# Optimization experiments

Measured on AMD Instinct MI355X. Metric: run time of the kernel, lower is better.

Reference implementation:

```python
import jax, jax.numpy as jnp
import numpy as np

NUM_HEADS = 4
NUM_GROUPS = 8
EPS = 1e-5


def setup_inputs() -> dict:
    key = jax.random.key(0)
    ks = jax.random.split(key, 4)
    b, c, h, w = 16, 512, 32, 32
    x = jax.random.normal(ks[0], (b, c, h, w), dtype=jnp.float32)
    gamma = jnp.ones((c,), dtype=jnp.float32)
    beta = jnp.zeros((c,), dtype=jnp.float32)
    # conv1d kernel-size-1 weights expressed as [out, in] matrices
    w_qkv = jax.random.normal(ks[1], (3 * c, c), dtype=jnp.float32) * (1.0 / np.sqrt(c))
    b_qkv = jnp.zeros((3 * c,), dtype=jnp.float32)
    w_proj = jax.random.normal(ks[2], (c, c), dtype=jnp.float32) * (1.0 / np.sqrt(c))
    b_proj = jnp.zeros((c,), dtype=jnp.float32)
    return {"x": x, "gamma": gamma, "beta": beta, "w_qkv": w_qkv,
            "b_qkv": b_qkv, "w_proj": w_proj, "b_proj": b_proj}


def group_norm(x, gamma, beta):
    # x: [b, c, h, w]; normalize per (group) over (c/g, h, w)
    b, c, h, w = x.shape
    xg = x.reshape(b, NUM_GROUPS, c // NUM_GROUPS, h, w)
    mean = xg.mean(axis=(2, 3, 4), keepdims=True)
    var = xg.var(axis=(2, 3, 4), keepdims=True)
    xn = ((xg - mean) * jax.lax.rsqrt(var + EPS)).reshape(b, c, h, w)
    return xn * gamma[None, :, None, None] + beta[None, :, None, None]


def reference(x, gamma, beta, w_qkv, b_qkv, w_proj, b_proj):
    b, c, h, w = x.shape
    L = h * w
    hd = c // NUM_HEADS  # head_dim
    x_in = x
    xn = group_norm(x, gamma, beta).reshape(b, c, L)
    # 1x1 conv == matmul over channel dim: [b, 3c, L]
    qkv = jnp.einsum('oc,bcl->bol', w_qkv, xn) + b_qkv[None, :, None]
    q, k, v = jnp.split(qkv, 3, axis=1)  # each [b, c, L]
    q = q.reshape(b, NUM_HEADS, hd, L)
    k = k.reshape(b, NUM_HEADS, hd, L)
    v = v.reshape(b, NUM_HEADS, hd, L)
    scale = hd ** (-0.5)
    attn = jnp.einsum('bhdl,bhdm->bhlm', q * scale, k)  # [b,h,L,L]
    attn = jax.nn.softmax(attn, axis=-1)
    out = jnp.einsum('bhlm,bhdm->bhdl', attn, v).reshape(b, c, L)
    out = jnp.einsum('oc,bcl->bol', w_proj, out) + b_proj[None, :, None]
    return x_in + out.reshape(b, c, h, w)
```

## Files before the change

kernel.cpp:

```cpp
#include <hip/hip_runtime.h>
#include <hip/hip_bf16.h>

typedef __hip_bfloat16 bf16;
typedef __attribute__((ext_vector_type(8))) short short8;
typedef __attribute__((ext_vector_type(4))) float f32x4;
typedef __attribute__((ext_vector_type(16))) float f32x16;

__device__ __forceinline__ float b2f(bf16 v) { return __bfloat162float(v); }
__device__ __forceinline__ bf16  f2b(float v) { return __float2bfloat16(v); }

__global__ __launch_bounds__(256) void convert_w_kernel(
    const float* __restrict__ wq, const float* __restrict__ wp,
    bf16* __restrict__ wqb, bf16* __restrict__ wpb)
{
    int ch = blockIdx.x * 256 + threadIdx.x;
    float4 v;
    bf16* dst;
    if (ch < 196608) {
        v = ((const float4*)wq)[ch];
        dst = wqb + ch * 4;
    } else {
        int c2 = ch - 196608;
        v = ((const float4*)wp)[c2];
        dst = wpb + c2 * 4;
    }
    bf16 o[4] = {f2b(v.x), f2b(v.y), f2b(v.z), f2b(v.w)};
    *(uint2*)dst = *(const uint2*)o;
}

__global__ __launch_bounds__(256) void gn_partial_kernel(
    const float* __restrict__ x,
    float* __restrict__ partS, float* __restrict__ partQ)
{
    const int bid = blockIdx.x;
    const size_t base = (size_t)bid * 16384;
    const int t = threadIdx.x;

    float sum = 0.f, ssq = 0.f;
    const float4* x4 = (const float4*)(x + base);
    for (int i = t; i < 4096; i += 256) {
        float4 v = x4[i];
        sum += v.x + v.y + v.z + v.w;
        ssq += v.x * v.x + v.y * v.y + v.z * v.z + v.w * v.w;
    }
    #pragma unroll
    for (int off = 32; off > 0; off >>= 1) {
        sum += __shfl_down(sum, off);
        ssq += __shfl_down(ssq, off);
    }
    __shared__ float red[8];
    const int wid = t >> 6, lane = t & 63;
    if (lane == 0) { red[wid] = sum; red[4 + wid] = ssq; }
    __syncthreads();
    if (t == 0) {
        partS[bid] = red[0] + red[1] + red[2] + red[3];
        partQ[bid] = red[4] + red[5] + red[6] + red[7];
    }
}

__global__ __launch_bounds__(64) void gn_finalize_kernel(
    const float* __restrict__ partS, const float* __restrict__ partQ,
    const float* __restrict__ gamma, const float* __restrict__ beta,
    float* __restrict__ scaleB, float* __restrict__ shiftB)
{
    const int bg = blockIdx.x;
    const int b = bg >> 3, g = bg & 7;
    const int t = threadIdx.x;
    float s = partS[bg * 4] + partS[bg * 4 + 1] + partS[bg * 4 + 2] + partS[bg * 4 + 3];
    float q = partQ[bg * 4] + partQ[bg * 4 + 1] + partQ[bg * 4 + 2] + partQ[bg * 4 + 3];
    float mean = s * (1.f / 65536.f);
    float var  = q * (1.f / 65536.f) - mean * mean;
    float rstd = rsqrtf(var + 1e-5f);
    int c = g * 64 + t;
    float sc = rstd * gamma[c];
    scaleB[b * 512 + c] = sc;
    shiftB[b * 512 + c] = beta[c] - mean * sc;
}

__global__ __launch_bounds__(256) void gn_apply_t_kernel(
    const float* __restrict__ x,
    const float* __restrict__ scaleB,
    const float* __restrict__ shiftB,
    bf16* __restrict__ Xt)
{
    const int lt = blockIdx.x, ct = blockIdx.y, b = blockIdx.z;
    const int l0 = lt * 64, c0 = ct * 64;
    const int t = threadIdx.x;
    __shared__ float Ls[64][65];

    const float* xb = x + ((size_t)b * 512 + c0) * 1024 + l0;
    for (int i = t; i < 1024; i += 256) {
        int cc = i >> 4, lc = (i & 15) * 4;
        float4 v = *(const float4*)(xb + (size_t)cc * 1024 + lc);
        float sc = scaleB[b * 512 + c0 + cc];
        float sh = shiftB[b * 512 + c0 + cc];
        Ls[cc][lc]     = v.x * sc + sh;
        Ls[cc][lc + 1] = v.y * sc + sh;
        Ls[cc][lc + 2] = v.z * sc + sh;
        Ls[cc][lc + 3] = v.w * sc + sh;
    }
    __syncthreads();
    for (int i = t; i < 1024; i += 256) {
        int l = i >> 4, cc = (i & 15) * 4;
        bf16 o[4] = {f2b(Ls[cc][l]), f2b(Ls[cc + 1][l]),
                     f2b(Ls[cc + 2][l]), f2b(Ls[cc + 3][l])};
        *(uint2*)(Xt + ((size_t)b * 1024 + l0 + l) * 512 + c0 + cc) = *(const uint2*)o;
    }
}

__global__ __launch_bounds__(256) void mfma_qkv_kernel(
    const bf16* __restrict__ W,
    const bf16* __restrict__ Xt,
    const float* __restrict__ bias,
    bf16* __restrict__ Qt,
    bf16* __restrict__ Kt,
    bf16* __restrict__ Vb)
{
    const int n0 = blockIdx.x * 128;
    const int m0 = blockIdx.y * 128;
    const int b  = blockIdx.z;
    const int t  = threadIdx.x;
    const int w  = t >> 6, lane = t & 63;
    const int c  = lane & 15, quad = lane >> 4;
    const int w0 = w & 1, w1 = w >> 1;
    const int ak = quad * 8;

    __shared__ __align__(16) bf16 smem[17408];
    bf16* As = smem;
    bf16* Bs = smem + 5120;
    bf16* Cs = smem;

    const bf16* Ag = W + (size_t)m0 * 512;
    const bf16* Bg = Xt + ((size_t)b * 1024 + n0) * 512;

    const int srow = t >> 2, skc = (t & 3) * 8;

    short8 areg[2], breg[2];
    #pragma unroll
    for (int it = 0; it < 2; it++) {
        int row = srow + it * 64;
        areg[it] = *(const short8*)(Ag + (size_t)row * 512 + skc);
        breg[it] = *(const short8*)(Bg + (size_t)row * 512 + skc);
    }

    f32x4 acc[4][4];
    #pragma unroll
    for (int i = 0; i < 4; i++)
        #pragma unroll
        for (int j = 0; j < 4; j++)
            #pragma unroll
            for (int r = 0; r < 4; r++) acc[i][j][r] = 0.f;

    for (int k0 = 0; k0 < 512; k0 += 32) {
        __syncthreads();
        #pragma unroll
        for (int it = 0; it < 2; it++) {
            int row = srow + it * 64;
            *(short8*)&As[row * 40 + skc] = areg[it];
            *(short8*)&Bs[row * 40 + skc] = breg[it];
        }
        __syncthreads();
        {
            int k1 = (k0 + 32) & 511;
            #pragma unroll
            for (int it = 0; it < 2; it++) {
                int row = srow + it * 64;
                areg[it] = *(const short8*)(Ag + (size_t)row * 512 + k1 + skc);
                breg[it] = *(const short8*)(Bg + (size_t)row * 512 + k1 + skc);
            }
        }
        short8 af[4], bf[4];
        #pragma unroll
        for (int jm = 0; jm < 4; jm++)
            af[jm] = *(const short8*)&As[(w0 * 64 + jm * 16 + c) * 40 + ak];
        #pragma unroll
        for (int jn = 0; jn < 4; jn++)
            bf[jn] = *(const short8*)&Bs[(w1 * 64 + jn * 16 + c) * 40 + ak];
        #pragma unroll
        for (int jm = 0; jm < 4; jm++)
            #pragma unroll
            for (int jn = 0; jn < 4; jn++)
                acc[jm][jn] = __builtin_amdgcn_mfma_f32_16x16x32_bf16(
                    af[jm], bf[jn], acc[jm][jn], 0, 0, 0);
    }

    __syncthreads();
    const int cls = m0 >> 9;
    if (cls < 2) {
        #pragma unroll
        for (int jm = 0; jm < 4; jm++) {
            #pragma unroll
            for (int jn = 0; jn < 4; jn++) {
                bf16 o4[4];
                #pragma unroll
                for (int r = 0; r < 4; r++) {
                    int orow = w0 * 64 + jm * 16 + quad * 4 + r;
                    o4[r] = f2b(acc[jm][jn][r] + bias[m0 + orow]);
                }
                *(uint2*)&Cs[(size_t)(w1 * 64 + jn * 16 + c) * 136
                             + w0 * 64 + jm * 16 + quad * 4] = *(const uint2*)o4;
            }
        }
        __syncthreads();
        const int head = (m0 >> 7) & 3;
        bf16* Db = (cls == 0 ? Qt : Kt)
                   + (((size_t)(b * 4 + head)) * 1024 + n0) * 128;
        for (int i = t; i < 2048; i += 256) {
            int row = i >> 4, ch = (i & 15) * 8;
            *(short8*)(Db + (size_t)row * 128 + ch) = *(const short8*)&Cs[row * 136 + ch];
        }
    } else {
        #pragma unroll
        for (int jm = 0; jm < 4; jm++) {
            #pragma unroll
            for (int r = 0; r < 4; r++) {
                int orow = w0 * 64 + jm * 16 + quad * 4 + r;
                float bs = bias[m0 + orow];
                #pragma unroll
                for (int jn = 0; jn < 4; jn++)
                    Cs[orow * 136 + w1 * 64 + jn * 16 + c] = f2b(acc[jm][jn][r] + bs);
            }
        }
        __syncthreads();
        bf16* Cb = Vb + ((size_t)b * 512 + (m0 - 1024)) * 1024 + n0;
        for (int i = t; i < 2048; i += 256) {
            int row = i >> 4, ch = (i & 15) * 8;
            *(short8*)(Cb + (size_t)row * 1024 + ch) = *(const short8*)&Cs[row * 136 + ch];
        }
    }
}

#define HD 128
#define QT 128
#define MT 64
#define SM_SHIFT 6.0f

__global__ __launch_bounds__(256, 2) void attn_mfma_kernel(
    const bf16* __restrict__ Qt,
    const bf16* __restrict__ Kt,
    const bf16* __restrict__ Vb,
    bf16* __restrict__ out)
{
    const int bh = blockIdx.x;
    const int qt = blockIdx.y;
    const int b = bh >> 2, h = bh & 3;
    const int t = threadIdx.x;
    const int w = t >> 6, lane = t & 63;
    const int wrow = lane & 31;
    const int blk  = lane >> 5;
    const int l0 = qt * QT;

    __shared__ __align__(16) bf16 smem[27136];
    bf16* Ks = smem;
    bf16* Vs = smem + 8704;
    bf16* Ps = smem + 17920;

    const int qrow = w * 32 + wrow;
    const bf16* Qr = Qt + (((size_t)(b * 4 + h)) * 1024 + l0 + qrow) * 128;
    short8 aq[8];
    #pragma unroll
    for (int kt = 0; kt < 8; kt++)
        aq[kt] = *(const short8*)(Qr + kt * 16 + blk * 8);

    const bf16* Kb = Kt + (((size_t)(b * 4 + h)) * 1024) * 128;
    const bf16* Vg = Vb + ((size_t)(b * 512 + h * HD)) * 1024;

    short8 kreg[4], vreg[4];
    #pragma unroll
    for (int p = 0; p < 4; p++) {
        int i = t + p * 256;
        kreg[p] = *(const short8*)(Kb + (size_t)(i >> 4) * 128 + (i & 15) * 8);
        vreg[p] = *(const short8*)(Vg + (size_t)(i >> 3) * 1024 + (i & 7) * 8);
    }

    f32x16 acc_o[4];
    #pragma unroll
    for (int n = 0; n < 4; n++)
        #pragma unroll
        for (int r = 0; r < 16; r++) acc_o[n][r] = 0.f;

    float psum[16];
    #pragma unroll
    for (int r = 0; r < 16; r++) psum[r] = 0.f;

    const float scale = 0.08838834764831845f;

    for (int mt = 0; mt < 1024 / MT; mt++) {
        __syncthreads();

        #pragma unroll
        for (int p = 0; p < 4; p++) {
            int i = t + p * 256;
            *(short8*)&Ks[(i >> 4) * 136 + (i & 15) * 8] = kreg[p];
            *(short8*)&Vs[(i >> 3) * 72 + (i & 7) * 8]   = vreg[p];
        }
        __syncthreads();

        {
            int m0n = (mt < 15) ? (mt + 1) * MT : 0;
            #pragma unroll
            for (int p = 0; p < 4; p++) {
                int i = t + p * 256;
                kreg[p] = *(const short8*)(Kb + (size_t)(m0n + (i >> 4)) * 128 + (i & 15) * 8);
                vreg[p] = *(const short8*)(Vg + (size_t)(i >> 3) * 1024 + m0n + (i & 7) * 8);
            }
        }

        f32x16 accs[2];
        #pragma unroll
        for (int n = 0; n < 2; n++)
            #pragma unroll
            for (int r = 0; r < 16; r++) accs[n][r] = 0.f;
        #pragma unroll
        for (int kt = 0; kt < 8; kt++) {
            #pragma unroll
            for (int nt = 0; nt < 2; nt++) {
                short8 bfr = *(const short8*)&Ks[(nt * 32 + wrow) * 136 + kt * 16 + blk * 8];
                accs[nt] = __builtin_amdgcn_mfma_f32_32x32x16_bf16(aq[kt], bfr, accs[nt], 0, 0, 0);
            }
        }

        #pragma unroll
        for (int nt = 0; nt < 2; nt++)
            #pragma unroll
            for (int r = 0; r < 16; r++) {
                float p = __expf(accs[nt][r] * scale - SM_SHIFT);
                psum[r] += p;
                int row = w * 32 + (r & 3) + 8 * (r >> 2) + 4 * blk;
                Ps[row * 72 + nt * 32 + wrow] = f2b(p);
            }

        #pragma unroll
        for (int kt2 = 0; kt2 < 4; kt2++) {
            short8 a = *(const short8*)&Ps[(w * 32 + wrow) * 72 + kt2 * 16 + blk * 8];
            #pragma unroll
            for (int nt2 = 0; nt2 < 4; nt2++) {
                short8 bv = *(const short8*)&Vs[(nt2 * 32 + wrow) * 72 + kt2 * 16 + blk * 8];
                acc_o[nt2] = __builtin_amdgcn_mfma_f32_32x32x16_bf16(a, bv, acc_o[nt2], 0, 0, 0);
            }
        }
    }

    #pragma unroll
    for (int off = 1; off < 32; off <<= 1)
        #pragma unroll
        for (int r = 0; r < 16; r++)
            psum[r] += __shfl_xor(psum[r], off);

    __syncthreads();
    bf16* Os = smem;
    float inv[16];
    #pragma unroll
    for (int r = 0; r < 16; r++) inv[r] = 1.f / psum[r];
    #pragma unroll
    for (int nt2 = 0; nt2 < 4; nt2++)
        #pragma unroll
        for (int r = 0; r < 16; r++) {
            int row = w * 32 + (r & 3) + 8 * (r >> 2) + 4 * blk;
            Os[row * 136 + nt2 * 32 + wrow] = f2b(acc_o[nt2][r] * inv[r]);
        }
    __syncthreads();
    bf16* Ob = out + ((size_t)b * 1024 + l0) * 512 + h * HD;
    for (int i = t; i < 2048; i += 256) {
        int row = i >> 4, ch = (i & 15) * 8;
        *(short8*)(Ob + (size_t)row * 512 + ch) = *(const short8*)&Os[row * 136 + ch];
    }
}

__global__ __launch_bounds__(256) void mfma_proj_kernel(
    const bf16* __restrict__ W,
    const bf16* __restrict__ Xt,
    const float* __restrict__ bias,
    const float* __restrict__ res,
    float* __restrict__ C)
{
    const int n0 = blockIdx.x * 128;
    const int m0 = blockIdx.y * 128;
    const int b  = blockIdx.z;
    const int t  = threadIdx.x;
    const int w  = t >> 6, lane = t & 63;
    const int c  = lane & 15, quad = lane >> 4;
    const int w0 = w & 1, w1 = w >> 1;
    const int ak = quad * 8;

    __shared__ __align__(16) bf16 smem[17408];
    bf16* As = smem;
    bf16* Bs = smem + 5120;
    bf16* Cs = smem;

    const bf16* Ag = W + (size_t)m0 * 512;
    const bf16* Bg = Xt + ((size_t)b * 1024 + n0) * 512;

    const int srow = t >> 2, skc = (t & 3) * 8;

    short8 areg[2], breg[2];
    #pragma unroll
    for (int it = 0; it < 2; it++) {
        int row = srow + it * 64;
        areg[it] = *(const short8*)(Ag + (size_t)row * 512 + skc);
        breg[it] = *(const short8*)(Bg + (size_t)row * 512 + skc);
    }

    f32x4 acc[4][4];
    #pragma unroll
    for (int i = 0; i < 4; i++)
        #pragma unroll
        for (int j = 0; j < 4; j++)
            #pragma unroll
            for (int r = 0; r < 4; r++) acc[i][j][r] = 0.f;

    for (int k0 = 0; k0 < 512; k0 += 32) {
        __syncthreads();
        #pragma unroll
        for (int it = 0; it < 2; it++) {
            int row = srow + it * 64;
            *(short8*)&As[row * 40 + skc] = areg[it];
            *(short8*)&Bs[row * 40 + skc] = breg[it];
        }
        __syncthreads();
        {
            int k1 = (k0 + 32) & 511;
            #pragma unroll
            for (int it = 0; it < 2; it++) {
                int row = srow + it * 64;
                areg[it] = *(const short8*)(Ag + (size_t)row * 512 + k1 + skc);
                breg[it] = *(const short8*)(Bg + (size_t)row * 512 + k1 + skc);
            }
        }
        short8 af[4], bf[4];
        #pragma unroll
        for (int jm = 0; jm < 4; jm++)
            af[jm] = *(const short8*)&As[(w0 * 64 + jm * 16 + c) * 40 + ak];
        #pragma unroll
        for (int jn = 0; jn < 4; jn++)
            bf[jn] = *(const short8*)&Bs[(w1 * 64 + jn * 16 + c) * 40 + ak];
        #pragma unroll
        for (int jm = 0; jm < 4; jm++)
            #pragma unroll
            for (int jn = 0; jn < 4; jn++)
                acc[jm][jn] = __builtin_amdgcn_mfma_f32_16x16x32_bf16(
                    af[jm], bf[jn], acc[jm][jn], 0, 0, 0);
    }

    __syncthreads();
    #pragma unroll
    for (int jm = 0; jm < 4; jm++) {
        #pragma unroll
        for (int r = 0; r < 4; r++) {
            int orow = w0 * 64 + jm * 16 + quad * 4 + r;
            float bs = bias[m0 + orow];
            #pragma unroll
            for (int jn = 0; jn < 4; jn++)
                Cs[orow * 136 + w1 * 64 + jn * 16 + c] = f2b(acc[jm][jn][r] + bs);
        }
    }
    __syncthreads();
    const float* Rb = res + ((size_t)b * 512 + m0) * 1024 + n0;
    float* Cb = C + ((size_t)b * 512 + m0) * 1024 + n0;
    for (int i = t; i < 4096; i += 256) {
        int row = i >> 5, ch = (i & 31) * 4;
        float4 rv = *(const float4*)(Rb + (size_t)row * 1024 + ch);
        float4 ov;
        ov.x = b2f(Cs[row * 136 + ch + 0]) + rv.x;
        ov.y = b2f(Cs[row * 136 + ch + 1]) + rv.y;
        ov.z = b2f(Cs[row * 136 + ch + 2]) + rv.z;
        ov.w = b2f(Cs[row * 136 + ch + 3]) + rv.w;
        *(float4*)(Cb + (size_t)row * 1024 + ch) = ov;
    }
}

extern "C" void kernel_launch(void* const* d_in, const int* in_sizes, int n_in,
                              void* d_out, int out_size, void* d_ws, size_t ws_size,
                              hipStream_t stream)
{
    const float* x      = (const float*)d_in[0];
    const float* gamma  = (const float*)d_in[1];
    const float* beta   = (const float*)d_in[2];
    const float* w_qkv  = (const float*)d_in[3];
    const float* b_qkv  = (const float*)d_in[4];
    const float* w_proj = (const float*)d_in[5];
    const float* b_proj = (const float*)d_in[6];
    float* out = (float*)d_out;

    char* ws = (char*)d_ws;
    float* scaleB = (float*)ws;
    float* shiftB = (float*)(ws + 32768);
    bf16*  wqb    = (bf16*)(ws + 65536);
    bf16*  wpb    = (bf16*)(ws + 65536 + 1572864);
    char*  big    = ws + 65536 + 2097152;
    bf16*  Xt     = (bf16*)(big);
    bf16*  Qt     = (bf16*)(big + (size_t)16777216);
    bf16*  Kt     = (bf16*)(big + (size_t)2 * 16777216);
    bf16*  Vb     = (bf16*)(big + (size_t)3 * 16777216);
    float* partS  = (float*)(big + (size_t)4 * 16777216);
    float* partQ  = partS + 512;
    bf16*  attn_t = Xt;

    hipLaunchKernelGGL(convert_w_kernel, dim3(1024), dim3(256), 0, stream,
                       w_qkv, w_proj, wqb, wpb);
    hipLaunchKernelGGL(gn_partial_kernel, dim3(512), dim3(256), 0, stream,
                       x, partS, partQ);
    hipLaunchKernelGGL(gn_finalize_kernel, dim3(128), dim3(64), 0, stream,
                       partS, partQ, gamma, beta, scaleB, shiftB);
    hipLaunchKernelGGL(gn_apply_t_kernel, dim3(16, 8, 16), dim3(256), 0, stream,
                       x, scaleB, shiftB, Xt);
    hipLaunchKernelGGL(mfma_qkv_kernel, dim3(8, 12, 16), dim3(256), 0, stream,
                       wqb, Xt, b_qkv, Qt, Kt, Vb);
    hipLaunchKernelGGL(attn_mfma_kernel, dim3(64, 8), dim3(256), 0, stream,
                       Qt, Kt, Vb, attn_t);
    hipLaunchKernelGGL(mfma_proj_kernel, dim3(8, 4, 16), dim3(256), 0, stream,
                       wpb, attn_t, b_proj, x, out);
}
```

Baseline: 228.0 us.

## Split attention key tile across two wave groups with shared-memory reduction

The attention kernel doubles its block to 512 threads. Each set of four waves computes scores and the PV product for one 32-key half of every 64-key tile, then the partial outputs and row sums are combined through shared memory before normalisation. This raises the number of waves available per CU and cuts per-wave register pressure, to hide MFMA and memory latency better. The cost is an extra cross-wave reduction with additional barriers and duplicated Q fragment loads.

```diff
diff --git a/kernel.cpp b/kernel.cpp
--- a/kernel.cpp
+++ b/kernel.cpp
@@ -235,7 +235,7 @@
 #define MT 64
 #define SM_SHIFT 6.0f
 
-__global__ __launch_bounds__(256, 2) void attn_mfma_kernel(
+__global__ __launch_bounds__(512, 4) void attn_mfma_kernel(
     const bf16* __restrict__ Qt,
     const bf16* __restrict__ Kt,
     const bf16* __restrict__ Vb,
@@ -245,7 +245,10 @@
     const int qt = blockIdx.y;
     const int b = bh >> 2, h = bh & 3;
     const int t = threadIdx.x;
-    const int w = t >> 6, lane = t & 63;
+    const int w8 = t >> 6;
+    const int w  = w8 & 3;
+    const int mh = w8 >> 2;
+    const int lane = t & 63;
     const int wrow = lane & 31;
     const int blk  = lane >> 5;
     const int l0 = qt * QT;
@@ -265,10 +268,10 @@
     const bf16* Kb = Kt + (((size_t)(b * 4 + h)) * 1024) * 128;
     const bf16* Vg = Vb + ((size_t)(b * 512 + h * HD)) * 1024;
 
-    short8 kreg[4], vreg[4];
-    #pragma unroll
-    for (int p = 0; p < 4; p++) {
-        int i = t + p * 256;
+    short8 kreg[2], vreg[2];
+    #pragma unroll
+    for (int p = 0; p < 2; p++) {
+        int i = t + p * 512;
         kreg[p] = *(const short8*)(Kb + (size_t)(i >> 4) * 128 + (i & 15) * 8);
         vreg[p] = *(const short8*)(Vg + (size_t)(i >> 3) * 1024 + (i & 7) * 8);
     }
@@ -289,8 +292,8 @@
         __syncthreads();
 
         #pragma unroll
-        for (int p = 0; p < 4; p++) {
-            int i = t + p * 256;
+        for (int p = 0; p < 2; p++) {
+            int i = t + p * 512;
             *(short8*)&Ks[(i >> 4) * 136 + (i & 15) * 8] = kreg[p];
             *(short8*)&Vs[(i >> 3) * 72 + (i & 7) * 8]   = vreg[p];
         }
@@ -299,43 +302,36 @@
         {
             int m0n = (mt < 15) ? (mt + 1) * MT : 0;
             #pragma unroll
-            for (int p = 0; p < 4; p++) {
-                int i = t + p * 256;
+            for (int p = 0; p < 2; p++) {
+                int i = t + p * 512;
                 kreg[p] = *(const short8*)(Kb + (size_t)(m0n + (i >> 4)) * 128 + (i & 15) * 8);
                 vreg[p] = *(const short8*)(Vg + (size_t)(i >> 3) * 1024 + m0n + (i & 7) * 8);
             }
         }
 
-        f32x16 accs[2];
-        #pragma unroll
-        for (int n = 0; n < 2; n++)
-            #pragma unroll
-            for (int r = 0; r < 16; r++) accs[n][r] = 0.f;
+        f32x16 accs;
+        #pragma unroll
+        for (int r = 0; r < 16; r++) accs[r] = 0.f;
         #pragma unroll
         for (int kt = 0; kt < 8; kt++) {
-            #pragma unroll
-            for (int nt = 0; nt < 2; nt++) {
-                short8 bfr = *(const short8*)&Ks[(nt * 32 + wrow) * 136 + kt * 16 + blk * 8];
-                accs[nt] = __builtin_amdgcn_mfma_f32_32x32x16_bf16(aq[kt], bfr, accs[nt], 0, 0, 0);
-            }
-        }
-
-        #pragma unroll
-        for (int nt = 0; nt < 2; nt++)
-            #pragma unroll
-            for (int r = 0; r < 16; r++) {
-                float p = __expf(accs[nt][r] * scale - SM_SHIFT);
-                psum[r] += p;
-                int row = w * 32 + (r & 3) + 8 * (r >> 2) + 4 * blk;
-                Ps[row * 72 + nt * 32 + wrow] = f2b(p);
-            }
-
-        #pragma unroll
-        for (int kt2 = 0; kt2 < 4; kt2++) {
-            short8 a = *(const short8*)&Ps[(w * 32 + wrow) * 72 + kt2 * 16 + blk * 8];
+            short8 bfr = *(const short8*)&Ks[(mh * 32 + wrow) * 136 + kt * 16 + blk * 8];
+            accs = __builtin_amdgcn_mfma_f32_32x32x16_bf16(aq[kt], bfr, accs, 0, 0, 0);
+        }
+
+        #pragma unroll
+        for (int r = 0; r < 16; r++) {
+            float p = __expf(accs[r] * scale - SM_SHIFT);
+            psum[r] += p;
+            int row = w * 32 + (r & 3) + 8 * (r >> 2) + 4 * blk;
+            Ps[row * 72 + mh * 32 + wrow] = f2b(p);
+        }
+
+        #pragma unroll
+        for (int kt2 = 0; kt2 < 2; kt2++) {
+            short8 a = *(const short8*)&Ps[(w * 32 + wrow) * 72 + (mh * 2 + kt2) * 16 + blk * 8];
             #pragma unroll
             for (int nt2 = 0; nt2 < 4; nt2++) {
-                short8 bv = *(const short8*)&Vs[(nt2 * 32 + wrow) * 72 + kt2 * 16 + blk * 8];
+                short8 bv = *(const short8*)&Vs[(nt2 * 32 + wrow) * 72 + (mh * 2 + kt2) * 16 + blk * 8];
                 acc_o[nt2] = __builtin_amdgcn_mfma_f32_32x32x16_bf16(a, bv, acc_o[nt2], 0, 0, 0);
             }
         }
@@ -347,21 +343,62 @@
         for (int r = 0; r < 16; r++)
             psum[r] += __shfl_xor(psum[r], off);
 
-    __syncthreads();
+    float* comb = (float*)smem;
+    float* psumArr = comb + 8704;
+    __syncthreads();
+
+    #pragma unroll
+    for (int half = 0; half < 2; half++) {
+        if (mh == 1) {
+            #pragma unroll
+            for (int n2 = 0; n2 < 2; n2++)
+                #pragma unroll
+                for (int r = 0; r < 16; r++) {
+                    int row = w * 32 + (r & 3) + 8 * (r >> 2) + 4 * blk;
+                    comb[row * 68 + n2 * 32 + wrow] = acc_o[half * 2 + n2][r];
+                }
+            if (half == 0 && wrow == 0)
+                #pragma unroll
+                for (int r = 0; r < 16; r++) {
+                    int row = w * 32 + (r & 3) + 8 * (r >> 2) + 4 * blk;
+                    psumArr[row] = psum[r];
+                }
+        }
+        __syncthreads();
+        if (mh == 0) {
+            #pragma unroll
+            for (int n2 = 0; n2 < 2; n2++)
+                #pragma unroll
+                for (int r = 0; r < 16; r++) {
+                    int row = w * 32 + (r & 3) + 8 * (r >> 2) + 4 * blk;
+                    acc_o[half * 2 + n2][r] += comb[row * 68 + n2 * 32 + wrow];
+                }
+            if (half == 0)
+                #pragma unroll
+                for (int r = 0; r < 16; r++) {
+                    int row = w * 32 + (r & 3) + 8 * (r >> 2) + 4 * blk;
+                    psum[r] += psumArr[row];
+                }
+        }
+        __syncthreads();
+    }
+
     bf16* Os = smem;
-    float inv[16];
-    #pragma unroll
-    for (int r = 0; r < 16; r++) inv[r] = 1.f / psum[r];
-    #pragma unroll
-    for (int nt2 = 0; nt2 < 4; nt2++)
-        #pragma unroll
-        for (int r = 0; r < 16; r++) {
-            int row = w * 32 + (r & 3) + 8 * (r >> 2) + 4 * blk;
-            Os[row * 136 + nt2 * 32 + wrow] = f2b(acc_o[nt2][r] * inv[r]);
-        }
+    if (mh == 0) {
+        float inv[16];
+        #pragma unroll
+        for (int r = 0; r < 16; r++) inv[r] = 1.f / psum[r];
+        #pragma unroll
+        for (int nt2 = 0; nt2 < 4; nt2++)
+            #pragma unroll
+            for (int r = 0; r < 16; r++) {
+                int row = w * 32 + (r & 3) + 8 * (r >> 2) + 4 * blk;
+                Os[row * 136 + nt2 * 32 + wrow] = f2b(acc_o[nt2][r] * inv[r]);
+            }
+    }
     __syncthreads();
     bf16* Ob = out + ((size_t)b * 1024 + l0) * 512 + h * HD;
-    for (int i = t; i < 2048; i += 256) {
+    for (int i = t; i < 2048; i += 512) {
         int row = i >> 4, ch = (i & 15) * 8;
         *(short8*)(Ob + (size_t)row * 512 + ch) = *(const short8*)&Os[row * 136 + ch];
     }
@@ -506,7 +543,7 @@
                        x, scaleB, shiftB, Xt);
     hipLaunchKernelGGL(mfma_qkv_kernel, dim3(8, 12, 16), dim3(256), 0, stream,
                        wqb, Xt, b_qkv, Qt, Kt, Vb);
-    hipLaunchKernelGGL(attn_mfma_kernel, dim3(64, 8), dim3(256), 0, stream,
+    hipLaunchKernelGGL(attn_mfma_kernel, dim3(64, 8), dim3(512), 0, stream,
                        Qt, Kt, Vb, attn_t);
     hipLaunchKernelGGL(mfma_proj_kernel, dim3(8, 4, 16), dim3(256), 0, stream,
                        wpb, attn_t, b_proj, x, out);
```

After: 267.5 us. 17.3% more time.
